# Performance work log

Measured on AMD Instinct MI355X. Metric: run time of the kernel, lower is better.

The kernel has to match this reference:

```python
import jax, jax.numpy as jnp
import numpy as np

K = 3  # spatial kernel size (TVConv_k_square == 9)


def setup_inputs() -> dict:
    key = jax.random.key(0)
    k1, k2 = jax.random.split(key)
    B, C, H, W = 8, 96, 128, 128
    x = jax.random.normal(k1, (B, C, H, W), dtype=jnp.float32)
    weight_maps = jax.random.normal(k2, (1, C, K, K, H, W), dtype=jnp.float32)
    return {"x": x, "weight_maps": weight_maps}


def reference(x, weight_maps):
    # Per-pixel spatially-varying 3x3 depthwise conv.
    B, C, H, W = x.shape
    xp = jnp.pad(x, ((0, 0), (0, 0), (1, 1), (1, 1)))  # zero pad, (B,C,H+2,W+2)
    # Gather the 9 shifted views (equivalent to the as_strided unfold, stride 1).
    patches = jnp.stack(
        [xp[:, :, i:i + H, j:j + W] for i in range(K) for j in range(K)], axis=2
    ).reshape(B, C, K, K, H, W)
    # Weighted sum over the 3x3 window per channel per pixel.
    out = (weight_maps * patches).sum(axis=(2, 3))  # (B,C,H,W)
    return out
```

## Files before the change

### kernel.cpp

```cpp
#include <hip/hip_runtime.h>
#include <hip/hip_bf16.h>


namespace {
constexpr int B = 8, C = 96, H = 128, W = 128;
constexpr int HW = H * W;
constexpr int TILES = C * (H / 8);
constexpr int S = 256;
constexpr int CHUNKS = TILES / S;
}

__global__ __launch_bounds__(256, 8) void tvconv_kernel(
    const float* __restrict__ x,
    const float* __restrict__ wm,
    float* __restrict__ out) {
  const int t    = threadIdx.x;
  const int s    = blockIdx.x & (S - 1);
  const int b    = blockIdx.x >> 8;
  const int tile = blockIdx.y * S + s;
  const int c    = tile >> 4;
  const int h    = (tile & 15) * 8 + (t >> 5);
  const int w    = (t & 31) * 4;

  const float* wp = wm + (size_t)c * 9 * HW + h * W + w;
  float4 wt[9];
#pragma unroll
  for (int k = 0; k < 9; ++k) {
    wt[k] = *reinterpret_cast<const float4*>(wp + (size_t)k * HW);
  }

  const float* xb = x + ((size_t)b * C + c) * HW + h * W + w;
  const float4 zero4 = make_float4(0.f, 0.f, 0.f, 0.f);
  float4 xr[3];
  xr[0] = (h > 0)     ? *reinterpret_cast<const float4*>(xb - W) : zero4;
  xr[1] = *reinterpret_cast<const float4*>(xb);
  xr[2] = (h < H - 1) ? *reinterpret_cast<const float4*>(xb + W) : zero4;

  const bool at_left  = ((t & 31) == 0);
  const bool at_right = ((t & 31) == 31);
  float acc[4] = {0.f, 0.f, 0.f, 0.f};
#pragma unroll
  for (int i = 0; i < 3; ++i) {
    const float4 ctr = xr[i];
    float left  = __shfl_up(ctr.w, 1);
    float right = __shfl_down(ctr.x, 1);
    if (at_left)  left  = 0.f;
    if (at_right) right = 0.f;
    const float xv[6] = {left, ctr.x, ctr.y, ctr.z, ctr.w, right};
#pragma unroll
    for (int j = 0; j < 3; ++j) {
      const float4 wv = wt[i * 3 + j];
      const float wa[4] = {wv.x, wv.y, wv.z, wv.w};
#pragma unroll
      for (int m = 0; m < 4; ++m) {
        acc[m] += wa[m] * xv[m + j];
      }
    }
  }

  float4 o;
  o.x = acc[0]; o.y = acc[1]; o.z = acc[2]; o.w = acc[3];
  *reinterpret_cast<float4*>(
      out + ((size_t)b * C + c) * HW + h * W + w) = o;
}

extern "C" void kernel_launch(void* const* d_in, const int* in_sizes, int n_in,
                              void* d_out, int out_size, void* d_ws, size_t ws_size,
                              hipStream_t stream) {
  const float* x  = (const float*)d_in[0];
  const float* wm = (const float*)d_in[1];
  float* out = (float*)d_out;

  dim3 grid(S * B, CHUNKS);
  tvconv_kernel<<<grid, dim3(256, 1, 1), 0, stream>>>(x, wm, out);
}
```

Baseline: 165.8 us.

## Loop batch inside block and stage x halo rows in LDS via async loads

Each block now handles one channel/8-row tile for all 8 batch images. It keeps the 9 per-pixel weights in registers and reuses them across the batch, instead of reloading weights once per batch element. The x rows with their halo are staged into LDS using global_load_lds direct-to-LDS loads, which removes the redundant row reads across threads. This gives a grid of only 1536 blocks with about 41KB of LDS each, lowering occupancy and parallelism in exchange for less weight traffic.

```diff
diff --git a/kernel.cpp b/kernel.cpp
--- a/kernel.cpp
+++ b/kernel.cpp
@@ -5,22 +5,40 @@
 namespace {
 constexpr int B = 8, C = 96, H = 128, W = 128;
 constexpr int HW = H * W;
-constexpr int TILES = C * (H / 8);
-constexpr int S = 256;
-constexpr int CHUNKS = TILES / S;
+constexpr int XROWS = 10;
+constexpr int XB = XROWS * W * 4;
 }
 
-__global__ __launch_bounds__(256, 8) void tvconv_kernel(
+typedef __attribute__((address_space(1))) void gbl_void;
+typedef __attribute__((address_space(3))) void lds_void;
+
+__global__ __launch_bounds__(256, 3) void tvconv_kernel(
     const float* __restrict__ x,
     const float* __restrict__ wm,
     float* __restrict__ out) {
-  const int t    = threadIdx.x;
-  const int s    = blockIdx.x & (S - 1);
-  const int b    = blockIdx.x >> 8;
-  const int tile = blockIdx.y * S + s;
-  const int c    = tile >> 4;
-  const int h    = (tile & 15) * 8 + (t >> 5);
-  const int w    = (t & 31) * 4;
+  __shared__ __align__(16) char xs[B * XB + 1024];
+
+  const int t  = threadIdx.x;
+  const int c  = blockIdx.x >> 4;
+  const int h0 = (blockIdx.x & 15) * 8;
+  const int lr = t >> 5;
+  const int w4 = t & 31;
+  const int h  = h0 + lr;
+  const int w  = w4 * 4;
+
+#pragma unroll
+  for (int k = 0; k < 10; ++k) {
+    const int i   = k * 256 + t;
+    const int b   = i / 320;
+    const int rem = i - b * 320;
+    const int r   = rem >> 5;
+    const int col = rem & 31;
+    int row = h0 - 1 + r;
+    row = min(max(row, 0), H - 1);
+    const float* src = x + ((size_t)(b * C + c)) * HW + row * W + col * 4;
+    __builtin_amdgcn_global_load_lds((const gbl_void*)src,
+                                     (lds_void*)(xs + i * 16), 16, 0, 0);
+  }
 
   const float* wp = wm + (size_t)c * 9 * HW + h * W + w;
   float4 wt[9];
@@ -29,39 +47,43 @@
     wt[k] = *reinterpret_cast<const float4*>(wp + (size_t)k * HW);
   }
 
-  const float* xb = x + ((size_t)b * C + c) * HW + h * W + w;
+  __syncthreads();
+
+  const bool at_left  = (w4 == 0);
+  const bool at_right = (w4 == 31);
+  const bool top_pad  = (h == 0);
+  const bool bot_pad  = (h == H - 1);
   const float4 zero4 = make_float4(0.f, 0.f, 0.f, 0.f);
-  float4 xr[3];
-  xr[0] = (h > 0)     ? *reinterpret_cast<const float4*>(xb - W) : zero4;
-  xr[1] = *reinterpret_cast<const float4*>(xb);
-  xr[2] = (h < H - 1) ? *reinterpret_cast<const float4*>(xb + W) : zero4;
 
-  const bool at_left  = ((t & 31) == 0);
-  const bool at_right = ((t & 31) == 31);
-  float acc[4] = {0.f, 0.f, 0.f, 0.f};
 #pragma unroll
-  for (int i = 0; i < 3; ++i) {
-    const float4 ctr = xr[i];
-    float left  = __shfl_up(ctr.w, 1);
-    float right = __shfl_down(ctr.x, 1);
-    if (at_left)  left  = 0.f;
-    if (at_right) right = 0.f;
-    const float xv[6] = {left, ctr.x, ctr.y, ctr.z, ctr.w, right};
+  for (int b = 0; b < B; ++b) {
+    float acc[4] = {0.f, 0.f, 0.f, 0.f};
 #pragma unroll
-    for (int j = 0; j < 3; ++j) {
-      const float4 wv = wt[i * 3 + j];
-      const float wa[4] = {wv.x, wv.y, wv.z, wv.w};
+    for (int i = 0; i < 3; ++i) {
+      float4 ctr = *reinterpret_cast<const float4*>(
+          xs + b * XB + (lr + i) * 512 + w4 * 16);
+      const bool pad = (i == 0 && top_pad) || (i == 2 && bot_pad);
+      if (pad) ctr = zero4;
+      float left  = __shfl_up(ctr.w, 1);
+      float right = __shfl_down(ctr.x, 1);
+      if (at_left)  left  = 0.f;
+      if (at_right) right = 0.f;
+      const float xv[6] = {left, ctr.x, ctr.y, ctr.z, ctr.w, right};
 #pragma unroll
-      for (int m = 0; m < 4; ++m) {
-        acc[m] += wa[m] * xv[m + j];
+      for (int j = 0; j < 3; ++j) {
+        const float4 wv = wt[i * 3 + j];
+        const float wa[4] = {wv.x, wv.y, wv.z, wv.w};
+#pragma unroll
+        for (int m = 0; m < 4; ++m) {
+          acc[m] += wa[m] * xv[m + j];
+        }
       }
     }
+    float4 o;
+    o.x = acc[0]; o.y = acc[1]; o.z = acc[2]; o.w = acc[3];
+    *reinterpret_cast<float4*>(
+        out + ((size_t)(b * C + c)) * HW + h * W + w) = o;
   }
-
-  float4 o;
-  o.x = acc[0]; o.y = acc[1]; o.z = acc[2]; o.w = acc[3];
-  *reinterpret_cast<float4*>(
-      out + ((size_t)b * C + c) * HW + h * W + w) = o;
 }
 
 extern "C" void kernel_launch(void* const* d_in, const int* in_sizes, int n_in,
@@ -71,6 +93,6 @@
   const float* wm = (const float*)d_in[1];
   float* out = (float*)d_out;
 
-  dim3 grid(S * B, CHUNKS);
-  tvconv_kernel<<<grid, dim3(256, 1, 1), 0, stream>>>(x, wm, out);
+  const int blocks = C * (H / 8);
+  tvconv_kernel<<<blocks, 256, 0, stream>>>(x, wm, out);
 }
```

Result: faster. 140.4 us (-15.3%).
